# Kernel optimization log

Hardware: AMD Instinct MI355X
Metric: run time of the kernel (lower is better)

Reference implementation:

```python
import jax, jax.numpy as jnp
import numpy as np

B, T, D_ENC, H, NUM_CLASSES = 256, 256, 512, 512, 96


def setup_inputs() -> dict:
    key = jax.random.key(0)
    ks = jax.random.split(key, 12)
    s = lambda k, shp, fan: jax.random.normal(k, shp, jnp.float32) / np.sqrt(fan)
    return {
        "prev_h": jax.random.normal(ks[0], (B, H), jnp.float32),
        "prev_c": jax.random.normal(ks[1], (B, H), jnp.float32),
        "batch_H": jax.random.normal(ks[2], (B, T, D_ENC), jnp.float32),
        "char_onehots": jax.random.uniform(ks[3], (B, NUM_CLASSES), jnp.float32),
        # i2h: Dense(D_ENC -> H, no bias); h2h: Dense(H -> H, bias); score: Dense(H -> 1, no bias)
        "Wi2h": s(ks[4], (D_ENC, H), D_ENC),
        "Wh2h": s(ks[5], (H, H), H),
        "bh2h": jnp.zeros((H,), jnp.float32),
        "Wscore": s(ks[6], (H, 1), H),
        # LSTMCell: input dim = D_ENC + NUM_CLASSES, gates [i, f, g, o]
        "Wk": s(ks[7], (D_ENC + NUM_CLASSES, 4 * H), D_ENC + NUM_CLASSES),
        "Uk": s(ks[8], (H, 4 * H), H),
        "bk": jnp.zeros((4 * H,), jnp.float32),
    }


def reference(prev_h, prev_c, batch_H, char_onehots, Wi2h, Wh2h, bh2h, Wscore, Wk, Uk, bk):
    # Bahdanau additive attention
    bH_proj = jnp.einsum('btd,dh->bth', batch_H, Wi2h)          # [B,T,H]
    h_proj = (prev_h @ Wh2h + bh2h)[:, None, :]                  # [B,1,H]
    e = jnp.tanh(bH_proj + h_proj) @ Wscore                      # [B,T,1]
    alpha = jax.nn.softmax(e, axis=1)                            # [B,T,1]
    context = jnp.einsum('bt,btd->bd', alpha[..., 0], batch_H)   # [B,D_enc]
    # LSTM cell step on [context ; char_onehots]
    x = jnp.concatenate([context, char_onehots], axis=1)         # [B, D_enc+num_classes]
    z = x @ Wk + prev_h @ Uk + bk                                # [B, 4H]
    i, f, g, o = jnp.split(z, 4, axis=1)
    c_new = jax.nn.sigmoid(f) * prev_c + jax.nn.sigmoid(i) * jnp.tanh(g)
    h_new = jax.nn.sigmoid(o) * jnp.tanh(c_new)
    return h_new, c_new, alpha
```

## Files before the change

### kernel.cpp

```cpp
#include <hip/hip_runtime.h>

typedef __bf16 bf16_t;
typedef bf16_t bf16x8 __attribute__((ext_vector_type(8)));
typedef unsigned short ushort8_t __attribute__((ext_vector_type(8)));
typedef unsigned short ushort4_t __attribute__((ext_vector_type(4)));
typedef float f32x4 __attribute__((ext_vector_type(4)));

__device__ __forceinline__ unsigned short f2bf(float f) {
    __bf16 h = (__bf16)f;
    return __builtin_bit_cast(unsigned short, h);
}
__device__ __forceinline__ float bf2f(unsigned short u) {
    union { unsigned int i; float f; } v; v.i = ((unsigned int)u) << 16; return v.f;
}
__device__ __forceinline__ float fast_tanh(float x) {
    float e2 = __expf(2.f * x);
    return 1.f - 2.f / (e2 + 1.f);
}
__device__ __forceinline__ float fast_sig(float x) {
    return 1.f / (1.f + __expf(-x));
}

__global__ void k0_wt2(const float* __restrict__ Wi2h, const float* __restrict__ Wh2h,
                       unsigned short* __restrict__ Wt, unsigned short* __restrict__ Wht) {
    __shared__ float tile[32][33];
    const float* W = blockIdx.z ? Wh2h : Wi2h;
    unsigned short* O = blockIdx.z ? Wht : Wt;
    int tx = threadIdx.x, ty = threadIdx.y;
    int bx = blockIdx.x, by = blockIdx.y;
#pragma unroll
    for (int j = 0; j < 4; ++j) {
        int r = by * 32 + ty + j * 8;
        int c = bx * 32 + tx;
        tile[ty + j * 8][tx] = W[r * 512 + c];
    }
    __syncthreads();
#pragma unroll
    for (int j = 0; j < 4; ++j) {
        int h = bx * 32 + ty + j * 8;
        int d = by * 32 + tx;
        O[h * 512 + d] = f2bf(tile[tx][ty + j * 8]);
    }
}

__global__ void k1x_conv(const float* __restrict__ src, unsigned short* __restrict__ dst) {
    int i = blockIdx.x * 256 + threadIdx.x;
    float4 f = ((const float4*)src)[i];
    ushort4_t u;
    u[0] = f2bf(f.x); u[1] = f2bf(f.y); u[2] = f2bf(f.z); u[3] = f2bf(f.w);
    ((ushort4_t*)dst)[i] = u;
}

__global__ void k1m_hproj(const unsigned short* __restrict__ ph_bf,
                          const unsigned short* __restrict__ Wht,
                          const float* __restrict__ bh2h,
                          float* __restrict__ h_proj) {
    int tid = threadIdx.x;
    int wave = tid >> 6, lane = tid & 63;
    int l15 = lane & 15, g = lane >> 4;
    int h0 = blockIdx.x * 64 + wave * 16;
    int m0 = blockIdx.y * 32;

    f32x4 acc[2];
    acc[0] = (f32x4){0.f, 0.f, 0.f, 0.f};
    acc[1] = (f32x4){0.f, 0.f, 0.f, 0.f};

    const unsigned short* abase = ph_bf + (size_t)(m0 + l15) * 512 + g * 8;
    const unsigned short* bbase = Wht + (size_t)(h0 + l15) * 512 + g * 8;
#pragma unroll
    for (int j = 0; j < 16; ++j) {
        bf16x8 bf = __builtin_bit_cast(bf16x8, *(const ushort8_t*)(bbase + j * 32));
        bf16x8 a0 = __builtin_bit_cast(bf16x8, *(const ushort8_t*)(abase + j * 32));
        bf16x8 a1 = __builtin_bit_cast(bf16x8, *(const ushort8_t*)(abase + 16 * 512 + j * 32));
        acc[0] = __builtin_amdgcn_mfma_f32_16x16x32_bf16(a0, bf, acc[0], 0, 0, 0);
        acc[1] = __builtin_amdgcn_mfma_f32_16x16x32_bf16(a1, bf, acc[1], 0, 0, 0);
    }
    int h = h0 + l15;
    float bias = bh2h[h];
#pragma unroll
    for (int mf = 0; mf < 2; ++mf)
#pragma unroll
        for (int r = 0; r < 4; ++r)
            h_proj[(size_t)(m0 + mf * 16 + g * 4 + r) * 512 + h] = acc[mf][r] + bias;
}

__global__ void k2x_conv(const float* __restrict__ src, unsigned short* __restrict__ dst) {
    int gid = blockIdx.x * 256 + threadIdx.x;
#pragma unroll 2
    for (int i = gid; i < 8388608; i += 4096 * 256) {
        float4 f = ((const float4*)src)[i];
        ushort4_t u;
        u[0] = f2bf(f.x); u[1] = f2bf(f.y); u[2] = f2bf(f.z); u[3] = f2bf(f.w);
        ((ushort4_t*)dst)[i] = u;
    }
}

__launch_bounds__(256, 2)
__global__ void k2b_scores(const unsigned short* __restrict__ bHb,
                           const unsigned short* __restrict__ Wt,
                           const float* __restrict__ h_proj,
                           const float* __restrict__ Wscore,
                           float* __restrict__ e_part) {
    __shared__ __align__(16) unsigned short Alds[8192];
    __shared__ __align__(16) unsigned short Blds[8192];
    __shared__ float hp_s[128];
    __shared__ float wsc_s[128];
    __shared__ float e_red[4][64];

    int tid = threadIdx.x;
    int wg = (blockIdx.x & 7) * 256 + (blockIdx.x >> 3);
    int mt = wg >> 2, nt = wg & 3;
    int m0 = mt * 128, n0 = nt * 128;
    int b  = m0 >> 8;

    if (tid < 128) hp_s[tid] = h_proj[(size_t)b * 512 + n0 + tid];
    else           wsc_s[tid - 128] = Wscore[n0 + tid - 128];

    int wave = tid >> 6;
    int lane = tid & 63;
    int wr = wave >> 1;
    int wc = wave & 1;
    int l15 = lane & 15, g = lane >> 4;
    int bchunk = ((lane & 7) ^ (lane >> 3)) << 3;
    int brow_l = lane >> 3;

    f32x4 acc[4][4];
#pragma unroll
    for (int mf = 0; mf < 4; ++mf)
#pragma unroll
        for (int nf = 0; nf < 4; ++nf)
            acc[mf][nf] = (f32x4){0.f, 0.f, 0.f, 0.f};

    for (int ks = 0; ks < 8; ++ks) {
        __syncthreads();
        int kbase = ks * 64;
#pragma unroll
        for (int i = 0; i < 4; ++i) {
            int q = wave * 4 + i;
            int row = q * 8 + brow_l;
            const unsigned short* gA = bHb + (size_t)(m0 + row) * 512 + kbase + bchunk;
            __builtin_amdgcn_global_load_lds(
                (const __attribute__((address_space(1))) void*)gA,
                (__attribute__((address_space(3))) void*)&Alds[q * 512], 16, 0, 0);
            const unsigned short* gB = Wt + (size_t)(n0 + row) * 512 + kbase + bchunk;
            __builtin_amdgcn_global_load_lds(
                (const __attribute__((address_space(1))) void*)gB,
                (__attribute__((address_space(3))) void*)&Blds[q * 512], 16, 0, 0);
        }
        __syncthreads();
#pragma unroll
        for (int kk = 0; kk < 2; ++kk) {
            bf16x8 af[4], bf[4];
#pragma unroll
            for (int mf = 0; mf < 4; ++mf) {
                int row = wr * 64 + mf * 16 + l15;
                int boff = row * 128 + ((((kk * 4 + g) ^ (l15 & 7))) << 4);
                af[mf] = __builtin_bit_cast(bf16x8, *(const ushort8_t*)((char*)Alds + boff));
            }
#pragma unroll
            for (int nf = 0; nf < 4; ++nf) {
                int row = wc * 64 + nf * 16 + l15;
                int boff = row * 128 + ((((kk * 4 + g) ^ (l15 & 7))) << 4);
                bf[nf] = __builtin_bit_cast(bf16x8, *(const ushort8_t*)((char*)Blds + boff));
            }
#pragma unroll
            for (int nf = 0; nf < 4; ++nf)
#pragma unroll
                for (int mf = 0; mf < 4; ++mf)
                    acc[mf][nf] = __builtin_amdgcn_mfma_f32_16x16x32_bf16(
                        af[mf], bf[nf], acc[mf][nf], 0, 0, 0);
        }
    }

    float s[4][4];
#pragma unroll
    for (int mf = 0; mf < 4; ++mf)
#pragma unroll
        for (int r = 0; r < 4; ++r) s[mf][r] = 0.f;

#pragma unroll
    for (int nf = 0; nf < 4; ++nf) {
        int nl = wc * 64 + nf * 16 + l15;
        float hpv = hp_s[nl], wv = wsc_s[nl];
#pragma unroll
        for (int mf = 0; mf < 4; ++mf)
#pragma unroll
            for (int r = 0; r < 4; ++r)
                s[mf][r] += wv * fast_tanh(acc[mf][nf][r] + hpv);
    }
#pragma unroll
    for (int mf = 0; mf < 4; ++mf)
#pragma unroll
        for (int r = 0; r < 4; ++r) {
            float v = s[mf][r];
            v += __shfl_xor(v, 1);
            v += __shfl_xor(v, 2);
            v += __shfl_xor(v, 4);
            v += __shfl_xor(v, 8);
            s[mf][r] = v;
        }
    if (l15 == 0) {
#pragma unroll
        for (int mf = 0; mf < 4; ++mf)
#pragma unroll
            for (int r = 0; r < 4; ++r)
                e_red[wave][mf * 16 + g * 4 + r] = s[mf][r];
    }
    __syncthreads();
    if (tid < 128) {
        int wrr = tid >> 6, i64 = tid & 63;
        float v = e_red[wrr * 2 + 0][i64] + e_red[wrr * 2 + 1][i64];
        e_part[(size_t)nt * 65536 + m0 + tid] = v;
    }
}

__launch_bounds__(256, 2)
__global__ void k2_scores(const float* __restrict__ batch_H,
                          const unsigned short* __restrict__ Wt,
                          const float* __restrict__ h_proj,
                          const float* __restrict__ Wscore,
                          float* __restrict__ e_part) {
    __shared__ __align__(16) unsigned short Alds[8192];
    __shared__ __align__(16) unsigned short Blds[8192];
    __shared__ float hp_s[128];
    __shared__ float wsc_s[128];
    __shared__ float e_red[4][64];

    int tid = threadIdx.x;
    int wg = (blockIdx.x & 7) * 256 + (blockIdx.x >> 3);
    int mt = wg >> 2, nt = wg & 3;
    int m0 = mt * 128, n0 = nt * 128;
    int b  = m0 >> 8;

    if (tid < 128) hp_s[tid] = h_proj[(size_t)b * 512 + n0 + tid];
    else           wsc_s[tid - 128] = Wscore[n0 + tid - 128];

    int wave = tid >> 6;
    int lane = tid & 63;
    int wr = wave >> 1;
    int wc = wave & 1;
    int l15 = lane & 15, g = lane >> 4;
    int bchunk = ((lane & 7) ^ (lane >> 3)) << 3;
    int brow_l = lane >> 3;

    f32x4 acc[4][4];
#pragma unroll
    for (int mf = 0; mf < 4; ++mf)
#pragma unroll
        for (int nf = 0; nf < 4; ++nf)
            acc[mf][nf] = (f32x4){0.f, 0.f, 0.f, 0.f};

    for (int ks = 0; ks < 8; ++ks) {
        __syncthreads();
        int kbase = ks * 64;
#pragma unroll
        for (int i = 0; i < 4; ++i) {
            int q = wave * 4 + i;
            int row = q * 8 + brow_l;
            const unsigned short* gsrc = Wt + (size_t)(n0 + row) * 512 + kbase + bchunk;
            __builtin_amdgcn_global_load_lds(
                (const __attribute__((address_space(1))) void*)gsrc,
                (__attribute__((address_space(3))) void*)&Blds[q * 512], 16, 0, 0);
        }
        float4 av[8];
#pragma unroll
        for (int j = 0; j < 8; ++j) {
            int idx = j * 256 + tid;
            int r = idx >> 4, c4 = idx & 15;
            av[j] = *(const float4*)(batch_H + (size_t)(m0 + r) * 512 + kbase + c4 * 4);
        }
#pragma unroll
        for (int j = 0; j < 8; ++j) {
            int idx = j * 256 + tid;
            int r = idx >> 4, c4 = idx & 15;
            ushort4_t u;
            u[0] = f2bf(av[j].x); u[1] = f2bf(av[j].y);
            u[2] = f2bf(av[j].z); u[3] = f2bf(av[j].w);
            int boff = r * 128 + ((((c4 >> 1) ^ (r & 7)) << 4) | ((c4 & 1) << 3));
            *(ushort4_t*)((char*)Alds + boff) = u;
        }
        __syncthreads();
#pragma unroll
        for (int kk = 0; kk < 2; ++kk) {
            bf16x8 af[4], bf[4];
#pragma unroll
            for (int mf = 0; mf < 4; ++mf) {
                int row = wr * 64 + mf * 16 + l15;
                int boff = row * 128 + ((((kk * 4 + g) ^ (l15 & 7))) << 4);
                af[mf] = __builtin_bit_cast(bf16x8, *(const ushort8_t*)((char*)Alds + boff));
            }
#pragma unroll
            for (int nf = 0; nf < 4; ++nf) {
                int row = wc * 64 + nf * 16 + l15;
                int boff = row * 128 + ((((kk * 4 + g) ^ (l15 & 7))) << 4);
                bf[nf] = __builtin_bit_cast(bf16x8, *(const ushort8_t*)((char*)Blds + boff));
            }
#pragma unroll
            for (int nf = 0; nf < 4; ++nf)
#pragma unroll
                for (int mf = 0; mf < 4; ++mf)
                    acc[mf][nf] = __builtin_amdgcn_mfma_f32_16x16x32_bf16(
                        af[mf], bf[nf], acc[mf][nf], 0, 0, 0);
        }
    }

    float s[4][4];
#pragma unroll
    for (int mf = 0; mf < 4; ++mf)
#pragma unroll
        for (int r = 0; r < 4; ++r) s[mf][r] = 0.f;

#pragma unroll
    for (int nf = 0; nf < 4; ++nf) {
        int nl = wc * 64 + nf * 16 + l15;
        float hpv = hp_s[nl], wv = wsc_s[nl];
#pragma unroll
        for (int mf = 0; mf < 4; ++mf)
#pragma unroll
            for (int r = 0; r < 4; ++r)
                s[mf][r] += wv * fast_tanh(acc[mf][nf][r] + hpv);
    }
#pragma unroll
    for (int mf = 0; mf < 4; ++mf)
#pragma unroll
        for (int r = 0; r < 4; ++r) {
            float v = s[mf][r];
            v += __shfl_xor(v, 1);
            v += __shfl_xor(v, 2);
            v += __shfl_xor(v, 4);
            v += __shfl_xor(v, 8);
            s[mf][r] = v;
        }
    if (l15 == 0) {
#pragma unroll
        for (int mf = 0; mf < 4; ++mf)
#pragma unroll
            for (int r = 0; r < 4; ++r)
                e_red[wave][mf * 16 + g * 4 + r] = s[mf][r];
    }
    __syncthreads();
    if (tid < 128) {
        int wrr = tid >> 6, i64 = tid & 63;
        float v = e_red[wrr * 2 + 0][i64] + e_red[wrr * 2 + 1][i64];
        e_part[(size_t)nt * 65536 + m0 + tid] = v;
    }
}

__global__ void k3_softmax(const float* __restrict__ e_part, float* __restrict__ alpha_out) {
    __shared__ float red[4];
    int b = blockIdx.x, tid = threadIdx.x;
    int m = b * 256 + tid;
    float v = e_part[m] + e_part[65536 + m] + e_part[131072 + m] + e_part[196608 + m];
    float mx = v;
#pragma unroll
    for (int off = 32; off; off >>= 1) mx = fmaxf(mx, __shfl_xor(mx, off));
    if ((tid & 63) == 0) red[tid >> 6] = mx;
    __syncthreads();
    mx = fmaxf(fmaxf(red[0], red[1]), fmaxf(red[2], red[3]));
    float p = __expf(v - mx);
    __syncthreads();
    float sum = p;
#pragma unroll
    for (int off = 32; off; off >>= 1) sum += __shfl_xor(sum, off);
    if ((tid & 63) == 0) red[tid >> 6] = sum;
    __syncthreads();
    sum = red[0] + red[1] + red[2] + red[3];
    alpha_out[b * 256 + tid] = p / sum;
}

__global__ void k4b_context(const unsigned short* __restrict__ bHb, const float* __restrict__ alpha,
                            unsigned short* __restrict__ xb) {
    __shared__ float al[256];
    int b = blockIdx.x, tid = threadIdx.x;
    al[tid] = alpha[b * 256 + tid];
    __syncthreads();
    const unsigned short* bh = bHb + (size_t)b * 256 * 512 + tid * 2;
    float a0 = 0.f, a1 = 0.f;
#pragma unroll 4
    for (int t = 0; t < 256; ++t) {
        unsigned int w = *(const unsigned int*)(bh + (size_t)t * 512);
        float av = al[t];
        a0 += av * bf2f((unsigned short)(w & 0xffff));
        a1 += av * bf2f((unsigned short)(w >> 16));
    }
    unsigned int p = (unsigned int)f2bf(a0) | ((unsigned int)f2bf(a1) << 16);
    *(unsigned int*)(&xb[(size_t)b * 1120 + tid * 2]) = p;
}

__global__ void k4_context(const float* __restrict__ batch_H, const float* __restrict__ alpha,
                           float* __restrict__ context) {
    __shared__ float al[256];
    int b = blockIdx.y, dc = blockIdx.x, tid = threadIdx.x;
    al[tid] = alpha[b * 256 + tid];
    __syncthreads();
    int d = dc * 256 + tid;
    const float* bh = batch_H + (size_t)b * 256 * 512 + d;
    float acc = 0.f;
#pragma unroll 4
    for (int t = 0; t < 256; ++t)
        acc += al[t] * bh[(size_t)t * 512];
    context[b * 512 + d] = acc;
}

__global__ void k5t_wzt(const float* __restrict__ Wk, const float* __restrict__ Uk,
                        unsigned short* __restrict__ Wzt) {
    __shared__ float tile[32][33];
    int tx = threadIdx.x, ty = threadIdx.y;
    int bx = blockIdx.x;
    int by = blockIdx.y;
#pragma unroll
    for (int j = 0; j < 4; ++j) {
        int k = bx * 32 + ty + j * 8;
        int c = by * 32 + tx;
        float v = (k < 608) ? Wk[(size_t)k * 2048 + c] : Uk[(size_t)(k - 608) * 2048 + c];
        tile[ty + j * 8][tx] = v;
    }
    __syncthreads();
#pragma unroll
    for (int j = 0; j < 4; ++j) {
        int n = by * 32 + ty + j * 8;
        int k = bx * 32 + tx;
        Wzt[(size_t)n * 1120 + k] = f2bf(tile[tx][ty + j * 8]);
    }
}

__global__ void k5x2_tail(const float* __restrict__ onehots, const float* __restrict__ prev_h,
                          unsigned short* __restrict__ xb) {
    int b = blockIdx.x, tid = threadIdx.x;
    for (int k = 512 + tid; k < 1120; k += 256) {
        float v = (k < 608) ? onehots[b * 96 + k - 512] : prev_h[b * 512 + k - 608];
        xb[(size_t)b * 1120 + k] = f2bf(v);
    }
}

__global__ void k5x_build(const float* __restrict__ context, const float* __restrict__ onehots,
                          const float* __restrict__ prev_h, unsigned short* __restrict__ xb) {
    int b = blockIdx.x, tid = threadIdx.x;
    for (int k = tid; k < 1120; k += 256) {
        float v;
        if (k < 512)      v = context[b * 512 + k];
        else if (k < 608) v = onehots[b * 96 + k - 512];
        else              v = prev_h[b * 512 + k - 608];
        xb[(size_t)b * 1120 + k] = f2bf(v);
    }
}

__launch_bounds__(256)
__global__ void k5m_fused(const unsigned short* __restrict__ xb,
                          const unsigned short* __restrict__ Wzt,
                          const float* __restrict__ bk,
                          const float* __restrict__ prev_c,
                          float* __restrict__ out) {
    __shared__ __align__(16) unsigned short Axs[32 * 232];

    int tid  = threadIdx.x;
    int wave = tid >> 6;
    int lane = tid & 63;
    int l15  = lane & 15;
    int g    = lane >> 4;
    int b0   = blockIdx.y * 32;
    int h0   = blockIdx.x * 64 + wave * 16;

    f32x4 acc[2][4];
#pragma unroll
    for (int mf = 0; mf < 2; ++mf)
#pragma unroll
        for (int gt = 0; gt < 4; ++gt)
            acc[mf][gt] = (f32x4){0.f, 0.f, 0.f, 0.f};

    const unsigned short* wbase = Wzt + (size_t)(h0 + l15) * 1120;

    for (int ks = 0; ks < 5; ++ks) {
        if (ks) __syncthreads();
        int kbase = ks * 224;
        for (int i = tid; i < 896; i += 256) {
            int row = i / 28;
            int c8  = (i % 28) * 8;
            *(ushort8_t*)(&Axs[row * 232 + c8]) =
                *(const ushort8_t*)(&xb[(size_t)(b0 + row) * 1120 + kbase + c8]);
        }
        __syncthreads();

        bf16x8 bcur[4], bnxt[4];
#pragma unroll
        for (int gt = 0; gt < 4; ++gt)
            bcur[gt] = __builtin_bit_cast(bf16x8,
                *(const ushort8_t*)(wbase + (size_t)gt * 512 * 1120 + kbase + g * 8));

#pragma unroll
        for (int kb = 0; kb < 7; ++kb) {
            if (kb < 6) {
                int kg = kbase + (kb + 1) * 32 + g * 8;
#pragma unroll
                for (int gt = 0; gt < 4; ++gt)
                    bnxt[gt] = __builtin_bit_cast(bf16x8,
                        *(const ushort8_t*)(wbase + (size_t)gt * 512 * 1120 + kg));
            }
            bf16x8 afrag[2];
#pragma unroll
            for (int mf = 0; mf < 2; ++mf)
                afrag[mf] = __builtin_bit_cast(bf16x8,
                    *(const ushort8_t*)(&Axs[(mf * 16 + l15) * 232 + kb * 32 + g * 8]));
#pragma unroll
            for (int gt = 0; gt < 4; ++gt)
#pragma unroll
                for (int mf = 0; mf < 2; ++mf)
                    acc[mf][gt] = __builtin_amdgcn_mfma_f32_16x16x32_bf16(
                        afrag[mf], bcur[gt], acc[mf][gt], 0, 0, 0);
#pragma unroll
            for (int gt = 0; gt < 4; ++gt) bcur[gt] = bnxt[gt];
        }
    }

    int h = h0 + l15;
    float bi = bk[h], bfv = bk[512 + h], bg = bk[1024 + h], bo = bk[1536 + h];
#pragma unroll
    for (int mf = 0; mf < 2; ++mf)
#pragma unroll
        for (int r = 0; r < 4; ++r) {
            int m = b0 + mf * 16 + g * 4 + r;
            float zi = acc[mf][0][r] + bi;
            float zf = acc[mf][1][r] + bfv;
            float zg = acc[mf][2][r] + bg;
            float zo = acc[mf][3][r] + bo;
            float c  = fast_sig(zf) * prev_c[m * 512 + h] + fast_sig(zi) * fast_tanh(zg);
            float hn = fast_sig(zo) * fast_tanh(c);
            out[m * 512 + h]          = hn;
            out[131072 + m * 512 + h] = c;
        }
}

extern "C" void kernel_launch(void* const* d_in, const int* in_sizes, int n_in,
                              void* d_out, int out_size, void* d_ws, size_t ws_size,
                              hipStream_t stream) {
    (void)in_sizes; (void)n_in; (void)out_size;
    const float* prev_h  = (const float*)d_in[0];
    const float* prev_c  = (const float*)d_in[1];
    const float* batch_H = (const float*)d_in[2];
    const float* onehots = (const float*)d_in[3];
    const float* Wi2h    = (const float*)d_in[4];
    const float* Wh2h    = (const float*)d_in[5];
    const float* bh2h    = (const float*)d_in[6];
    const float* Wscore  = (const float*)d_in[7];
    const float* Wk      = (const float*)d_in[8];
    const float* Uk      = (const float*)d_in[9];
    const float* bk      = (const float*)d_in[10];
    float* out = (float*)d_out;
    float* alpha = out + 262144;

    char* ws = (char*)d_ws;

    if (ws_size >= 70565888) {
        unsigned short* bHb   = (unsigned short*)(ws + 0);
        unsigned short* Wt    = (unsigned short*)(ws + 67108864);
        unsigned short* Wht   = (unsigned short*)(ws + 67633152);
        unsigned short* ph_bf = (unsigned short*)(ws + 68157440);
        float*          h_proj= (float*)(ws + 68419584);
        float*          e_part= (float*)(ws + 68943872);
        unsigned short* xb    = (unsigned short*)(ws + 69992448);
        unsigned short* Wzt   = (unsigned short*)(ws + 0);

        k0_wt2    <<<dim3(16, 16, 2), dim3(32, 8), 0, stream>>>(Wi2h, Wh2h, Wt, Wht);
        k1x_conv  <<<128, 256, 0, stream>>>(prev_h, ph_bf);
        k1m_hproj <<<dim3(8, 8), 256, 0, stream>>>(ph_bf, Wht, bh2h, h_proj);
        k2x_conv  <<<4096, 256, 0, stream>>>(batch_H, bHb);
        k2b_scores<<<2048, 256, 0, stream>>>(bHb, Wt, h_proj, Wscore, e_part);
        k3_softmax<<<256, 256, 0, stream>>>(e_part, alpha);
        k4b_context<<<256, 256, 0, stream>>>(bHb, alpha, xb);
        k5x2_tail <<<256, 256, 0, stream>>>(onehots, prev_h, xb);
        k5t_wzt   <<<dim3(35, 64), dim3(32, 8), 0, stream>>>(Wk, Uk, Wzt);
        k5m_fused <<<dim3(8, 8), 256, 0, stream>>>(xb, Wzt, bk, prev_c, out);
    } else {
        unsigned short* Wt     = (unsigned short*)(ws + 0);
        unsigned short* Wht    = (unsigned short*)(ws + 524288);
        unsigned short* ph_bf  = (unsigned short*)(ws + 1048576);
        float*          h_proj = (float*)(ws + 1310720);
        float*          e_part = (float*)(ws + 1835008);
        unsigned short* Wzt    = (unsigned short*)(ws + 0);
        unsigned short* xb     = (unsigned short*)(ws + 4587520);
        float*          context= (float*)(ws + 5160960);

        k0_wt2    <<<dim3(16, 16, 2), dim3(32, 8), 0, stream>>>(Wi2h, Wh2h, Wt, Wht);
        k1x_conv  <<<128, 256, 0, stream>>>(prev_h, ph_bf);
        k1m_hproj <<<dim3(8, 8), 256, 0, stream>>>(ph_bf, Wht, bh2h, h_proj);
        k2_scores <<<2048, 256, 0, stream>>>(batch_H, Wt, h_proj, Wscore, e_part);
        k3_softmax<<<256, 256, 0, stream>>>(e_part, alpha);
        k4_context<<<dim3(2, 256), 256, 0, stream>>>(batch_H, alpha, context);
        k5t_wzt   <<<dim3(35, 64), dim3(32, 8), 0, stream>>>(Wk, Uk, Wzt);
        k5x_build <<<256, 256, 0, stream>>>(context, onehots, prev_h, xb);
        k5m_fused <<<dim3(8, 8), 256, 0, stream>>>(xb, Wzt, bk, prev_c, out);
    }
}
```

Measured before the change: 162.0 us.

## Pipeline scores GEMM with 3-stage LDS ring and 256x128 tiles

Replaces the bf16 scores GEMM kernel with an 8-wave version that uses 256x128 tiles, one block per batch row-block, and a triple-buffered LDS ring filled by async global-to-LDS loads. Loads for later k-steps are issued while MFMAs run, with vmcnt waits, raw barriers and setprio around the MFMA bursts. The goal is to hide global memory latency and halve the re-reads of the B operand. In exchange it uses about 147KB of LDS, so only one block fits per CU, and the manual waitcnt bookkeeping is fragile.

```diff
diff --git a/kernel.cpp b/kernel.cpp
--- a/kernel.cpp
+++ b/kernel.cpp
@@ -95,122 +95,151 @@
     }
 }
 
-__launch_bounds__(256, 2)
-__global__ void k2b_scores(const unsigned short* __restrict__ bHb,
-                           const unsigned short* __restrict__ Wt,
-                           const float* __restrict__ h_proj,
-                           const float* __restrict__ Wscore,
-                           float* __restrict__ e_part) {
-    __shared__ __align__(16) unsigned short Alds[8192];
-    __shared__ __align__(16) unsigned short Blds[8192];
+__device__ __forceinline__ void k2b8_stage(int u, int m0, int n0, int wave, int lane,
+                                           const unsigned short* bHb, const unsigned short* Wt,
+                                           char* ring_) {
+    int ts = u / 6, us = u % 6, slot = ts % 3, kbase = ts * 64;
+    int rsub = wave * 8 + (lane >> 3);
+    int schunk = ((lane & 7) ^ (lane >> 3)) << 3;
+    const unsigned short* src;
+    char* dst;
+    if (us < 4) {
+        src = bHb + (size_t)(m0 + us * 64 + rsub) * 512 + kbase + schunk;
+        dst = ring_ + slot * 49152 + us * 8192 + wave * 1024;
+    } else {
+        src = Wt + (size_t)(n0 + (us - 4) * 64 + rsub) * 512 + kbase + schunk;
+        dst = ring_ + slot * 49152 + 32768 + (us - 4) * 8192 + wave * 1024;
+    }
+    __builtin_amdgcn_global_load_lds((const __attribute__((address_space(1))) void*)src,
+                                     (__attribute__((address_space(3))) void*)dst, 16, 0, 0);
+}
+
+__launch_bounds__(512, 1)
+__global__ void k2b8_scores(const unsigned short* __restrict__ bHb,
+                            const unsigned short* __restrict__ Wt,
+                            const float* __restrict__ h_proj,
+                            const float* __restrict__ Wscore,
+                            float* __restrict__ e_part) {
+    __shared__ __align__(16) char ring_[3 * 49152];
     __shared__ float hp_s[128];
     __shared__ float wsc_s[128];
-    __shared__ float e_red[4][64];
+    __shared__ float e_red[4][256];
 
     int tid = threadIdx.x;
-    int wg = (blockIdx.x & 7) * 256 + (blockIdx.x >> 3);
+    int wg = (blockIdx.x & 7) * 128 + (blockIdx.x >> 3);
     int mt = wg >> 2, nt = wg & 3;
-    int m0 = mt * 128, n0 = nt * 128;
-    int b  = m0 >> 8;
-
-    if (tid < 128) hp_s[tid] = h_proj[(size_t)b * 512 + n0 + tid];
-    else           wsc_s[tid - 128] = Wscore[n0 + tid - 128];
+    int m0 = mt * 256, n0 = nt * 128;
+
+    if (tid < 128) hp_s[tid] = h_proj[(size_t)mt * 512 + n0 + tid];
+    else if (tid < 256) wsc_s[tid - 128] = Wscore[n0 + tid - 128];
 
     int wave = tid >> 6;
     int lane = tid & 63;
-    int wr = wave >> 1;
-    int wc = wave & 1;
+    int wr = wave >> 2;
+    int wc = wave & 3;
     int l15 = lane & 15, g = lane >> 4;
-    int bchunk = ((lane & 7) ^ (lane >> 3)) << 3;
-    int brow_l = lane >> 3;
-
-    f32x4 acc[4][4];
-#pragma unroll
-    for (int mf = 0; mf < 4; ++mf)
-#pragma unroll
-        for (int nf = 0; nf < 4; ++nf)
-            acc[mf][nf] = (f32x4){0.f, 0.f, 0.f, 0.f};
-
-    for (int ks = 0; ks < 8; ++ks) {
-        __syncthreads();
-        int kbase = ks * 64;
-#pragma unroll
-        for (int i = 0; i < 4; ++i) {
-            int q = wave * 4 + i;
-            int row = q * 8 + brow_l;
-            const unsigned short* gA = bHb + (size_t)(m0 + row) * 512 + kbase + bchunk;
-            __builtin_amdgcn_global_load_lds(
-                (const __attribute__((address_space(1))) void*)gA,
-                (__attribute__((address_space(3))) void*)&Alds[q * 512], 16, 0, 0);
-            const unsigned short* gB = Wt + (size_t)(n0 + row) * 512 + kbase + bchunk;
-            __builtin_amdgcn_global_load_lds(
-                (const __attribute__((address_space(1))) void*)gB,
-                (__attribute__((address_space(3))) void*)&Blds[q * 512], 16, 0, 0);
-        }
-        __syncthreads();
+
+    f32x4 acc[8][2];
+#pragma unroll
+    for (int mr = 0; mr < 8; ++mr)
+#pragma unroll
+        for (int nr = 0; nr < 2; ++nr)
+            acc[mr][nr] = (f32x4){0.f, 0.f, 0.f, 0.f};
+
+#pragma unroll
+    for (int u = 0; u < 12; ++u)
+        k2b8_stage(u, m0, n0, wave, lane, bHb, Wt, ring_);
+    asm volatile("s_waitcnt vmcnt(6)" ::: "memory");
+    __builtin_amdgcn_s_barrier();
+
+#pragma unroll
+    for (int p = 0; p < 16; ++p) {
+        const int t = p >> 1, q = p & 1, slot = t % 3;
+        const char* Abase = ring_ + slot * 49152;
+        const char* Bbase = Abase + 32768;
+
+        bf16x8 af[4][2], bf[2][2];
 #pragma unroll
         for (int kk = 0; kk < 2; ++kk) {
-            bf16x8 af[4], bf[4];
-#pragma unroll
-            for (int mf = 0; mf < 4; ++mf) {
-                int row = wr * 64 + mf * 16 + l15;
-                int boff = row * 128 + ((((kk * 4 + g) ^ (l15 & 7))) << 4);
-                af[mf] = __builtin_bit_cast(bf16x8, *(const ushort8_t*)((char*)Alds + boff));
+#pragma unroll
+            for (int mr = 0; mr < 4; ++mr) {
+                int arow = wr * 128 + q * 64 + mr * 16 + l15;
+                af[mr][kk] = __builtin_bit_cast(bf16x8,
+                    *(const ushort8_t*)(Abase + arow * 128 + (((kk * 4 + g) ^ (arow & 7)) << 4)));
             }
 #pragma unroll
-            for (int nf = 0; nf < 4; ++nf) {
-                int row = wc * 64 + nf * 16 + l15;
-                int boff = row * 128 + ((((kk * 4 + g) ^ (l15 & 7))) << 4);
-                bf[nf] = __builtin_bit_cast(bf16x8, *(const ushort8_t*)((char*)Blds + boff));
+            for (int nr = 0; nr < 2; ++nr) {
+                int brow = wc * 32 + nr * 16 + l15;
+                bf[nr][kk] = __builtin_bit_cast(bf16x8,
+                    *(const ushort8_t*)(Bbase + brow * 128 + (((kk * 4 + g) ^ (brow & 7)) << 4)));
             }
-#pragma unroll
-            for (int nf = 0; nf < 4; ++nf)
-#pragma unroll
-                for (int mf = 0; mf < 4; ++mf)
-                    acc[mf][nf] = __builtin_amdgcn_mfma_f32_16x16x32_bf16(
-                        af[mf], bf[nf], acc[mf][nf], 0, 0, 0);
-        }
-    }
-
-    float s[4][4];
-#pragma unroll
-    for (int mf = 0; mf < 4; ++mf)
-#pragma unroll
-        for (int r = 0; r < 4; ++r) s[mf][r] = 0.f;
-
-#pragma unroll
-    for (int nf = 0; nf < 4; ++nf) {
-        int nl = wc * 64 + nf * 16 + l15;
+        }
+
+#pragma unroll
+        for (int i = 0; i < 3; ++i) {
+            int u = 3 * p + 12 + i;
+            if (u < 48) k2b8_stage(u, m0, n0, wave, lane, bHb, Wt, ring_);
+        }
+
+        if (q == 1) {
+            if (t < 6) asm volatile("s_waitcnt vmcnt(6)" ::: "memory");
+            else       asm volatile("s_waitcnt vmcnt(0)" ::: "memory");
+        }
+        __builtin_amdgcn_s_barrier();
+        asm volatile("s_waitcnt lgkmcnt(0)" ::: "memory");
+        __builtin_amdgcn_sched_barrier(0);
+
+        __builtin_amdgcn_s_setprio(1);
+#pragma unroll
+        for (int nr = 0; nr < 2; ++nr)
+#pragma unroll
+            for (int mr = 0; mr < 4; ++mr)
+#pragma unroll
+                for (int kk = 0; kk < 2; ++kk)
+                    acc[q * 4 + mr][nr] = __builtin_amdgcn_mfma_f32_16x16x32_bf16(
+                        af[mr][kk], bf[nr][kk], acc[q * 4 + mr][nr], 0, 0, 0);
+        __builtin_amdgcn_s_setprio(0);
+        __builtin_amdgcn_s_barrier();
+    }
+
+    float s[8][4];
+#pragma unroll
+    for (int mr = 0; mr < 8; ++mr)
+#pragma unroll
+        for (int r = 0; r < 4; ++r) s[mr][r] = 0.f;
+
+#pragma unroll
+    for (int nr = 0; nr < 2; ++nr) {
+        int nl = wc * 32 + nr * 16 + l15;
         float hpv = hp_s[nl], wv = wsc_s[nl];
 #pragma unroll
-        for (int mf = 0; mf < 4; ++mf)
+        for (int mr = 0; mr < 8; ++mr)
 #pragma unroll
             for (int r = 0; r < 4; ++r)
-                s[mf][r] += wv * fast_tanh(acc[mf][nf][r] + hpv);
-    }
-#pragma unroll
-    for (int mf = 0; mf < 4; ++mf)
+                s[mr][r] += wv * fast_tanh(acc[mr][nr][r] + hpv);
+    }
+#pragma unroll
+    for (int mr = 0; mr < 8; ++mr)
 #pragma unroll
         for (int r = 0; r < 4; ++r) {
-            float v = s[mf][r];
+            float v = s[mr][r];
             v += __shfl_xor(v, 1);
             v += __shfl_xor(v, 2);
             v += __shfl_xor(v, 4);
             v += __shfl_xor(v, 8);
-            s[mf][r] = v;
+            s[mr][r] = v;
         }
     if (l15 == 0) {
 #pragma unroll
-        for (int mf = 0; mf < 4; ++mf)
+        for (int mr = 0; mr < 8; ++mr)
 #pragma unroll
             for (int r = 0; r < 4; ++r)
-                e_red[wave][mf * 16 + g * 4 + r] = s[mf][r];
-    }
-    __syncthreads();
-    if (tid < 128) {
-        int wrr = tid >> 6, i64 = tid & 63;
-        float v = e_red[wrr * 2 + 0][i64] + e_red[wrr * 2 + 1][i64];
-        e_part[(size_t)nt * 65536 + m0 + tid] = v;
+                e_red[wc][wr * 128 + mr * 16 + g * 4 + r] = s[mr][r];
+    }
+    __syncthreads();
+    if (tid < 256) {
+        e_part[(size_t)nt * 65536 + m0 + tid] =
+            e_red[0][tid] + e_red[1][tid] + e_red[2][tid] + e_red[3][tid];
     }
 }
 
@@ -282,7 +311,7 @@
         __syncthreads();
 #pragma unroll
         for (int kk = 0; kk < 2; ++kk) {
-            bf16x8 af[4], bf[4];
+            bf16x8 af[4], bfr[4];
 #pragma unroll
             for (int mf = 0; mf < 4; ++mf) {
                 int row = wr * 64 + mf * 16 + l15;
@@ -293,14 +322,14 @@
             for (int nf = 0; nf < 4; ++nf) {
                 int row = wc * 64 + nf * 16 + l15;
                 int boff = row * 128 + ((((kk * 4 + g) ^ (l15 & 7))) << 4);
-                bf[nf] = __builtin_bit_cast(bf16x8, *(const ushort8_t*)((char*)Blds + boff));
+                bfr[nf] = __builtin_bit_cast(bf16x8, *(const ushort8_t*)((char*)Blds + boff));
             }
 #pragma unroll
             for (int nf = 0; nf < 4; ++nf)
 #pragma unroll
                 for (int mf = 0; mf < 4; ++mf)
                     acc[mf][nf] = __builtin_amdgcn_mfma_f32_16x16x32_bf16(
-                        af[mf], bf[nf], acc[mf][nf], 0, 0, 0);
+                        af[mf], bfr[nf], acc[mf][nf], 0, 0, 0);
         }
     }
 
@@ -560,16 +589,16 @@
         unsigned short* xb    = (unsigned short*)(ws + 69992448);
         unsigned short* Wzt   = (unsigned short*)(ws + 0);
 
-        k0_wt2    <<<dim3(16, 16, 2), dim3(32, 8), 0, stream>>>(Wi2h, Wh2h, Wt, Wht);
-        k1x_conv  <<<128, 256, 0, stream>>>(prev_h, ph_bf);
-        k1m_hproj <<<dim3(8, 8), 256, 0, stream>>>(ph_bf, Wht, bh2h, h_proj);
-        k2x_conv  <<<4096, 256, 0, stream>>>(batch_H, bHb);
-        k2b_scores<<<2048, 256, 0, stream>>>(bHb, Wt, h_proj, Wscore, e_part);
-        k3_softmax<<<256, 256, 0, stream>>>(e_part, alpha);
+        k0_wt2     <<<dim3(16, 16, 2), dim3(32, 8), 0, stream>>>(Wi2h, Wh2h, Wt, Wht);
+        k1x_conv   <<<128, 256, 0, stream>>>(prev_h, ph_bf);
+        k1m_hproj  <<<dim3(8, 8), 256, 0, stream>>>(ph_bf, Wht, bh2h, h_proj);
+        k2x_conv   <<<4096, 256, 0, stream>>>(batch_H, bHb);
+        k2b8_scores<<<1024, 512, 0, stream>>>(bHb, Wt, h_proj, Wscore, e_part);
+        k3_softmax <<<256, 256, 0, stream>>>(e_part, alpha);
         k4b_context<<<256, 256, 0, stream>>>(bHb, alpha, xb);
-        k5x2_tail <<<256, 256, 0, stream>>>(onehots, prev_h, xb);
-        k5t_wzt   <<<dim3(35, 64), dim3(32, 8), 0, stream>>>(Wk, Uk, Wzt);
-        k5m_fused <<<dim3(8, 8), 256, 0, stream>>>(xb, Wzt, bk, prev_c, out);
+        k5x2_tail  <<<256, 256, 0, stream>>>(onehots, prev_h, xb);
+        k5t_wzt    <<<dim3(35, 64), dim3(32, 8), 0, stream>>>(Wk, Uk, Wzt);
+        k5m_fused  <<<dim3(8, 8), 256, 0, stream>>>(xb, Wzt, bk, prev_c, out);
     } else {
         unsigned short* Wt     = (unsigned short*)(ws + 0);
         unsigned short* Wht    = (unsigned short*)(ws + 524288);
```

Result: slower. 174.4 us (+7.7%).
